# Optimization experiments

Hardware: AMD Instinct MI355X
Metric: run time of the kernel (lower is better)

## Reference

```python
import jax, jax.numpy as jnp
import numpy as np

# dims matching init_kwargs / input_specs
N, C, H, W = 8, 256, 64, 64
OUT_C, KH, KW = 256, 3, 3
STRIDE, PAD = 1, 1
OUT_H = (H - KH + 2 * PAD) // STRIDE + 1  # 64
OUT_W = (W - KW + 2 * PAD) // STRIDE + 1  # 64
K = KH * KW


def setup_inputs() -> dict:
    key = jax.random.key(0)
    k1, k2, k3 = jax.random.split(key, 3)
    x = jax.random.normal(k1, (N, C, H, W), dtype=jnp.float32)
    offset = jax.random.normal(k2, (N, 2 * K, OUT_H, OUT_W), dtype=jnp.float32)
    # kaiming-uniform-ish scale for weight (fan_in = C*KH*KW)
    bound = 1.0 / np.sqrt(C * KH * KW)
    weight = jax.random.uniform(k3, (OUT_C, C, KH, KW), dtype=jnp.float32,
                                minval=-bound, maxval=bound)
    return {"input": x, "offset": offset, "weight": weight}


def _deform_conv(x, offset, weight):
    # base sampling positions in pixel coords: y = oy*stride + ky - pad
    ky = jnp.repeat(jnp.arange(KH, dtype=jnp.float32) - PAD, KW)  # [K]
    kx = jnp.tile(jnp.arange(KW, dtype=jnp.float32) - PAD, KH)    # [K]
    oy = jnp.arange(OUT_H, dtype=jnp.float32) * STRIDE            # [outH]
    ox = jnp.arange(OUT_W, dtype=jnp.float32) * STRIDE            # [outW]
    base_y = ky[:, None, None] + oy[None, :, None]  # [K, outH, 1]
    base_x = kx[:, None, None] + ox[None, None, :]  # [K, 1, outW]

    off = offset.reshape(N, K, 2, OUT_H, OUT_W)
    y = base_y[None] + off[:, :, 0]  # [N, K, outH, outW], offset channel 0 = dy
    xp = base_x[None] + off[:, :, 1]  # channel 1 = dx

    # bilinear sample with zero padding (grid_sample align_corners=True, zeros)
    y0 = jnp.floor(y)
    x0 = jnp.floor(xp)
    bidx = jnp.arange(N)[:, None, None, None]
    acc = jnp.zeros((N, K, OUT_H, OUT_W, C), dtype=x.dtype)
    for dy in (0.0, 1.0):
        for dx in (0.0, 1.0):
            yi = y0 + dy
            xi = x0 + dx
            wgt = (1.0 - jnp.abs(y - yi)) * (1.0 - jnp.abs(xp - xi))
            valid = ((yi >= 0) & (yi <= H - 1) & (xi >= 0) & (xi <= W - 1))
            yc = jnp.clip(yi, 0, H - 1).astype(jnp.int32)
            xc = jnp.clip(xi, 0, W - 1).astype(jnp.int32)
            g = x[bidx, :, yc, xc]  # [N, K, outH, outW, C]
            acc = acc + g * (wgt * valid.astype(x.dtype))[..., None]

    # weight.view(outC, -1) flattens (C, KH, KW) -> (C, K) ordering
    w = weight.reshape(OUT_C, C, K)
    out = jnp.einsum('nkhwc,ock->nohw', acc, w)  # [N, outC, outH, outW]
    return out


def reference(input, offset, weight):
    # NOTE: original forward never adds bias -> faithfully omitted
    return _deform_conv(input, offset, weight)
```

## Files before the change

### kernel.cpp

```cpp
#include <hip/hip_runtime.h>
#include <hip/hip_fp16.h>
#include <stdint.h>


typedef _Float16 half8 __attribute__((ext_vector_type(8)));
typedef float f32x4 __attribute__((ext_vector_type(4)));

__device__ __forceinline__ __half2 h2(uint32_t u) {
  return __builtin_bit_cast(__half2, u);
}
__device__ __forceinline__ uint32_t packh2f(float a, float b) {
  return __builtin_bit_cast(uint32_t, __floats2half2_rn(a, b));
}
__device__ __forceinline__ __half2 duplo(uint32_t u) {
  return __half2half2(__builtin_bit_cast(__half, (unsigned short)(u & 0xffffu)));
}
__device__ __forceinline__ __half2 duphi(uint32_t u) {
  return __half2half2(__builtin_bit_cast(__half, (unsigned short)(u >> 16)));
}

__global__ __launch_bounds__(256) void prep_all_kernel(
    const float* __restrict__ x, const float* __restrict__ w,
    const float* __restrict__ offset,
    unsigned short* __restrict__ xb, unsigned short* __restrict__ w3s,
    unsigned short* __restrict__ coords) {
  __shared__ float tile[64][65];
  int tid = threadIdx.x;
  if (blockIdx.x < 2048) {
    int bn   = blockIdx.x >> 8;
    int rem  = blockIdx.x & 255;
    int y    = rem >> 2;
    int cblk = rem & 3;
    const float* src = x + ((size_t)(bn * 256 + cblk * 64)) * 4096 + y * 64;
#pragma unroll
    for (int i = 0; i < 4; ++i) {
      int u  = i * 256 + tid;
      int cl = u >> 4;
      int xs = (u & 15) * 4;
      float4 v = *(const float4*)(src + cl * 4096 + xs);
      tile[cl][xs] = v.x; tile[cl][xs + 1] = v.y;
      tile[cl][xs + 2] = v.z; tile[cl][xs + 3] = v.w;
    }
    __syncthreads();
    unsigned short* dst = xb + ((size_t)(bn * 64 + y) * 64) * 256 + cblk * 64;
#pragma unroll
    for (int i = 0; i < 8; ++i) {
      int v2  = i * 256 + tid;
      int xc  = v2 >> 5;
      int cl2 = (v2 & 31) * 2;
      *(uint32_t*)(dst + xc * 256 + cl2) = packh2f(tile[cl2][xc], tile[cl2 + 1][xc]);
    }
  } else if (blockIdx.x < 4352) {
    int idx = (blockIdx.x - 2048) * 256 + tid;
    int t    = idx >> 14;
    int r2   = idx & 16383;
    int e    = r2 & 7;
    int lane = (r2 >> 3) & 63;
    int ks   = (r2 >> 9) & 1;
    int nn   = (r2 >> 10) & 3;
    int wcol = (r2 >> 12) & 3;
    int oc = wcol * 64 + nn * 16 + (lane & 15);
    int kk = (ks * 4 + (lane >> 4)) * 8 + e;
    int c  = (t & 3) * 64 + kk;
    int k  = t >> 2;
    w3s[idx] = __builtin_bit_cast(unsigned short, __float2half(w[(oc * 256 + c) * 9 + k]));
  } else {
    int idx = (blockIdx.x - 4352) * 256 + tid;
    int ow  = idx & 63;
    int oh  = (idx >> 6) & 63;
    int r   = idx >> 12;
    int k   = r % 9;
    int bn  = r / 9;
    int ky = k / 3 - 1;
    int kx = k % 3 - 1;
    float offy = offset[((bn * 18 + 2 * k    ) * 64 + oh) * 64 + ow];
    float offx = offset[((bn * 18 + 2 * k + 1) * 64 + oh) * 64 + ow];
    float y = (float)(oh + ky) + offy;
    float x2 = (float)(ow + kx) + offx;
    float y0f = floorf(y), x0f = floorf(x2);
    float fy = y - y0f, fx = x2 - x0f;
    int y0 = (int)y0f, x0 = (int)x0f;
    int y1 = y0 + 1, x1 = x0 + 1;
    float vy0 = (y0 >= 0 && y0 <= 63) ? 1.0f : 0.0f;
    float vy1 = (y1 >= 0 && y1 <= 63) ? 1.0f : 0.0f;
    float vx0 = (x0 >= 0 && x0 <= 63) ? 1.0f : 0.0f;
    float vx1 = (x1 >= 0 && x1 <= 63) ? 1.0f : 0.0f;
    float wy0 = (1.0f - fy) * vy0, wy1 = fy * vy1;
    float wx0 = (1.0f - fx) * vx0, wx1 = fx * vx1;
    int y0c = min(max(y0, 0), 63), y1c = min(max(y1, 0), 63);
    int x0c = min(max(x0, 0), 63), x1c = min(max(x1, 0), 63);
    unsigned short ent[8];
    ent[0] = __builtin_bit_cast(unsigned short, __float2half(wy0 * wx0));
    ent[1] = __builtin_bit_cast(unsigned short, __float2half(wy0 * wx1));
    ent[2] = __builtin_bit_cast(unsigned short, __float2half(wy1 * wx0));
    ent[3] = __builtin_bit_cast(unsigned short, __float2half(wy1 * wx1));
    ent[4] = (unsigned short)(y0c * 64 + x0c);
    ent[5] = (unsigned short)(y0c * 64 + x1c);
    ent[6] = (unsigned short)(y1c * 64 + x0c);
    ent[7] = (unsigned short)(y1c * 64 + x1c);
    *(uint4*)(coords + (size_t)idx * 8) = *(const uint4*)ent;
  }
}

__global__ __launch_bounds__(512, 2) void deform_mfma_kernel(
    const unsigned short* __restrict__ xb,
    const unsigned short* __restrict__ coords,
    const unsigned short* __restrict__ w3s,
    float* __restrict__ out) {
  __shared__ __align__(16) unsigned short At[2][128 * 64];

  int bn  = blockIdx.x & 7;
  int ohp = blockIdx.x >> 3;
  int tid = threadIdx.x;

  int w    = tid >> 6;
  int lane = tid & 63;
  int wrow = w & 1;
  int wcol = w >> 1;
  int mrow = lane & 15;
  int quad = lane >> 4;

  int srow = tid >> 3;
  int sg   = tid & 7;

  const char* xbc = (const char*)(xb + (size_t)bn * (64 * 64 * 256));
  const unsigned short* cb0 = coords + ((size_t)((bn * 9) * 64 + ohp * 2) * 64 + srow) * 8;
  const unsigned short* cb1 = cb0 + 512;

  int aw0  = srow * 64 + ((sg ^ (srow & 7)) * 8);
  int grp0 = quad ^ (mrow & 7);
  int grp1 = (4 + quad) ^ (mrow & 7);
  int a_base = (wrow * 64 + mrow) * 64;
  int b_off  = wcol * 8192 + lane * 16;

  f32x4 acc[4][4] = {};
  half8 bA[2][4], bB[2][4];

  __half2 w00, w01, w02, w03, w10, w11, w12, w13;
  uint32_t o00, o01, o02, o03, o10, o11, o12, o13;
  uint4 cn0, cn1;
  uint4 ga0, ga1, ga2, ga3, gb0, gb1, gb2, gb3;

#define CBAR()                                                                  \
  {                                                                             \
    asm volatile("s_waitcnt lgkmcnt(0)" ::: "memory");                          \
    __builtin_amdgcn_s_barrier();                                               \
    asm volatile("" ::: "memory");                                              \
  }

#define BLOADR(TT, BS)                                                          \
  {                                                                             \
    const char* wp = (const char*)w3s + (size_t)(TT) * 32768 + b_off;           \
    _Pragma("unroll")                                                           \
    for (int nn = 0; nn < 4; ++nn) {                                            \
      BS[0][nn] = *(const half8*)(wp + (nn * 2 + 0) * 1024);                    \
      BS[1][nn] = *(const half8*)(wp + (nn * 2 + 1) * 1024);                    \
    }                                                                           \
  }

#define TAPSETUP_R(CE0, CE1)                                                    \
  {                                                                             \
    w00 = duplo((CE0).x); w01 = duphi((CE0).x);                                 \
    w02 = duplo((CE0).y); w03 = duphi((CE0).y);                                 \
    o00 = (((CE0).z & 0xffffu) << 9) + sg * 16;                                 \
    o01 = (((CE0).z >> 16) << 9) + sg * 16;                                     \
    o02 = (((CE0).w & 0xffffu) << 9) + sg * 16;                                 \
    o03 = (((CE0).w >> 16) << 9) + sg * 16;                                     \
    w10 = duplo((CE1).x); w11 = duphi((CE1).x);                                 \
    w12 = duplo((CE1).y); w13 = duphi((CE1).y);                                 \
    o10 = (((CE1).z & 0xffffu) << 9) + sg * 16;                                 \
    o11 = (((CE1).z >> 16) << 9) + sg * 16;                                     \
    o12 = (((CE1).w & 0xffffu) << 9) + sg * 16;                                 \
    o13 = (((CE1).w >> 16) << 9) + sg * 16;                                     \
  }

#define AGATHER(TT)                                                             \
  {                                                                             \
    ga0 = *(const uint4*)(xbc + o00 + ((TT) & 3) * 128);                        \
    ga1 = *(const uint4*)(xbc + o01 + ((TT) & 3) * 128);                        \
    ga2 = *(const uint4*)(xbc + o02 + ((TT) & 3) * 128);                        \
    ga3 = *(const uint4*)(xbc + o03 + ((TT) & 3) * 128);                        \
    gb0 = *(const uint4*)(xbc + o10 + ((TT) & 3) * 128);                        \
    gb1 = *(const uint4*)(xbc + o11 + ((TT) & 3) * 128);                        \
    gb2 = *(const uint4*)(xbc + o12 + ((TT) & 3) * 128);                        \
    gb3 = *(const uint4*)(xbc + o13 + ((TT) & 3) * 128);                        \
  }

#define AMATH(ATP)                                                              \
  {                                                                             \
    __half2 r0 = __hmul2(h2(ga0.x), w00);                                       \
    r0 = __hfma2(h2(ga1.x), w01, r0); r0 = __hfma2(h2(ga2.x), w02, r0);         \
    r0 = __hfma2(h2(ga3.x), w03, r0);                                           \
    __half2 r1 = __hmul2(h2(ga0.y), w00);                                       \
    r1 = __hfma2(h2(ga1.y), w01, r1); r1 = __hfma2(h2(ga2.y), w02, r1);         \
    r1 = __hfma2(h2(ga3.y), w03, r1);                                           \
    __half2 r2 = __hmul2(h2(ga0.z), w00);                                       \
    r2 = __hfma2(h2(ga1.z), w01, r2); r2 = __hfma2(h2(ga2.z), w02, r2);         \
    r2 = __hfma2(h2(ga3.z), w03, r2);                                           \
    __half2 r3 = __hmul2(h2(ga0.w), w00);                                       \
    r3 = __hfma2(h2(ga1.w), w01, r3); r3 = __hfma2(h2(ga2.w), w02, r3);         \
    r3 = __hfma2(h2(ga3.w), w03, r3);                                           \
    uint4 pk;                                                                   \
    pk.x = __builtin_bit_cast(uint32_t, r0);                                    \
    pk.y = __builtin_bit_cast(uint32_t, r1);                                    \
    pk.z = __builtin_bit_cast(uint32_t, r2);                                    \
    pk.w = __builtin_bit_cast(uint32_t, r3);                                    \
    *(uint4*)((ATP) + aw0) = pk;                                                \
    __half2 s0 = __hmul2(h2(gb0.x), w10);                                       \
    s0 = __hfma2(h2(gb1.x), w11, s0); s0 = __hfma2(h2(gb2.x), w12, s0);         \
    s0 = __hfma2(h2(gb3.x), w13, s0);                                           \
    __half2 s1 = __hmul2(h2(gb0.y), w10);                                       \
    s1 = __hfma2(h2(gb1.y), w11, s1); s1 = __hfma2(h2(gb2.y), w12, s1);         \
    s1 = __hfma2(h2(gb3.y), w13, s1);                                           \
    __half2 s2 = __hmul2(h2(gb0.z), w10);                                       \
    s2 = __hfma2(h2(gb1.z), w11, s2); s2 = __hfma2(h2(gb2.z), w12, s2);         \
    s2 = __hfma2(h2(gb3.z), w13, s2);                                           \
    __half2 s3 = __hmul2(h2(gb0.w), w10);                                       \
    s3 = __hfma2(h2(gb1.w), w11, s3); s3 = __hfma2(h2(gb2.w), w12, s3);         \
    s3 = __hfma2(h2(gb3.w), w13, s3);                                           \
    uint4 qk;                                                                   \
    qk.x = __builtin_bit_cast(uint32_t, s0);                                    \
    qk.y = __builtin_bit_cast(uint32_t, s1);                                    \
    qk.z = __builtin_bit_cast(uint32_t, s2);                                    \
    qk.w = __builtin_bit_cast(uint32_t, s3);                                    \
    *(uint4*)((ATP) + aw0 + 4096) = qk;                                         \
  }

#define COMPUTE(ATP, BS)                                                        \
  {                                                                             \
    __builtin_amdgcn_s_setprio(1);                                              \
    _Pragma("unroll")                                                           \
    for (int m = 0; m < 4; ++m) {                                               \
      half8 af0 = *(const half8*)((ATP) + a_base + m * 1024 + grp0 * 8);        \
      half8 af1 = *(const half8*)((ATP) + a_base + m * 1024 + grp1 * 8);        \
      _Pragma("unroll")                                                         \
      for (int nn = 0; nn < 4; ++nn) {                                          \
        acc[m][nn] = __builtin_amdgcn_mfma_f32_16x16x32_f16(af0, BS[0][nn], acc[m][nn], 0, 0, 0); \
        acc[m][nn] = __builtin_amdgcn_mfma_f32_16x16x32_f16(af1, BS[1][nn], acc[m][nn], 0, 0, 0); \
      }                                                                         \
    }                                                                           \
    __builtin_amdgcn_s_setprio(0);                                              \
  }

  {
    uint4 ce0 = *(const uint4*)cb0;
    uint4 ce1 = *(const uint4*)cb1;
    TAPSETUP_R(ce0, ce1)
  }
  AGATHER(0)
  BLOADR(0, bA)
  AMATH(&At[0][0])
  CBAR()

  for (int tap = 0; tap < 9; ++tap) {
#pragma unroll
    for (int cc = 0; cc < 4; ++cc) {
      const int t = tap * 4 + cc;
      if (t < 35) {
        if (cc == 3) TAPSETUP_R(cn0, cn1)
        AGATHER(t + 1)
        if (cc == 2 && tap < 8) {
          cn0 = *(const uint4*)(cb0 + (tap + 1) * 32768);
          cn1 = *(const uint4*)(cb1 + (tap + 1) * 32768);
        }
        if (cc & 1) { BLOADR(t + 1, bA) } else { BLOADR(t + 1, bB) }
      }
      if (cc & 1) { COMPUTE(&At[1][0], bB) } else { COMPUTE(&At[0][0], bA) }
      if (t < 35) {
        if (cc & 1) { AMATH(&At[0][0]) } else { AMATH(&At[1][0]) }
      }
      CBAR()
    }
  }

  float* outp = out + (size_t)bn * 256 * 4096 + (size_t)(ohp * 2 + wrow) * 64;
#pragma unroll
  for (int m = 0; m < 4; ++m) {
    int ow0 = m * 16 + quad * 4;
#pragma unroll
    for (int nn = 0; nn < 4; ++nn) {
      int oc = wcol * 64 + nn * 16 + mrow;
      *(f32x4*)(outp + (size_t)oc * 4096 + ow0) = acc[m][nn];
    }
  }
#undef CBAR
#undef BLOADR
#undef TAPSETUP_R
#undef AGATHER
#undef AMATH
#undef COMPUTE
}

extern "C" void kernel_launch(void* const* d_in, const int* in_sizes, int n_in,
                              void* d_out, int out_size, void* d_ws, size_t ws_size,
                              hipStream_t stream) {
  (void)in_sizes; (void)n_in; (void)out_size; (void)ws_size;
  const float* x      = (const float*)d_in[0];
  const float* offset = (const float*)d_in[1];
  const float* weight = (const float*)d_in[2];
  float* out = (float*)d_out;

  unsigned short* xb     = (unsigned short*)d_ws;
  unsigned short* w3s    = xb + (size_t)8 * 64 * 64 * 256;
  unsigned short* coords = w3s + (size_t)36 * 16384;

  prep_all_kernel<<<5504, 256, 0, stream>>>(x, weight, offset, xb, w3s, coords);
  deform_mfma_kernel<<<256, 512, 0, stream>>>(xb, coords, w3s, out);
}
```

Before: 140.7 us.

## Stage weight tiles into LDS via global_load_lds with double buffering

Weight (B) tiles were previously loaded straight from global memory into registers by every wave. They are now copied asynchronously into a double-buffered LDS tile with global_load_lds, each wave moving a slice, and then read from LDS into fragments just before the MFMAs. Explicit vmcnt waits replace the implicit register dependency. This removes redundant global traffic per wave and frees registers. In exchange it adds LDS reads, raises LDS usage (which may limit occupancy at 2 blocks per CU), and relies on the hand-counted vmcnt values being correct.

After: 149.9 us. 6.5% more time.

```diff
diff --git a/kernel.cpp b/kernel.cpp
--- a/kernel.cpp
+++ b/kernel.cpp
@@ -108,6 +108,7 @@
     const unsigned short* __restrict__ w3s,
     float* __restrict__ out) {
   __shared__ __align__(16) unsigned short At[2][128 * 64];
+  __shared__ __align__(16) unsigned short Bt[2][16384];
 
   int bn  = blockIdx.x & 7;
   int ohp = blockIdx.x >> 3;
@@ -131,10 +132,10 @@
   int grp0 = quad ^ (mrow & 7);
   int grp1 = (4 + quad) ^ (mrow & 7);
   int a_base = (wrow * 64 + mrow) * 64;
-  int b_off  = wcol * 8192 + lane * 16;
+  int b_off  = wcol * 4096 + lane * 8;
+  int d_off  = w * 2048 + lane * 8;
 
   f32x4 acc[4][4] = {};
-  half8 bA[2][4], bB[2][4];
 
   __half2 w00, w01, w02, w03, w10, w11, w12, w13;
   uint32_t o00, o01, o02, o03, o10, o11, o12, o13;
@@ -148,13 +149,16 @@
     asm volatile("" ::: "memory");                                              \
   }
 
-#define BLOADR(TT, BS)                                                          \
-  {                                                                             \
-    const char* wp = (const char*)w3s + (size_t)(TT) * 32768 + b_off;           \
+#define BDMA(TT, BB)                                                            \
+  {                                                                             \
+    const unsigned short* src = w3s + (size_t)(TT) * 16384 + d_off;             \
+    unsigned short* dst = &Bt[BB][0] + w * 2048;                                \
     _Pragma("unroll")                                                           \
-    for (int nn = 0; nn < 4; ++nn) {                                            \
-      BS[0][nn] = *(const half8*)(wp + (nn * 2 + 0) * 1024);                    \
-      BS[1][nn] = *(const half8*)(wp + (nn * 2 + 1) * 1024);                    \
+    for (int j = 0; j < 4; ++j) {                                               \
+      __builtin_amdgcn_global_load_lds(                                         \
+          (const __attribute__((address_space(1))) void*)(src + j * 512),       \
+          (__attribute__((address_space(3))) void*)(dst + j * 512),             \
+          16, 0, 0);                                                            \
     }                                                                           \
   }
 
@@ -226,8 +230,21 @@
     *(uint4*)((ATP) + aw0 + 4096) = qk;                                         \
   }
 
-#define COMPUTE(ATP, BS)                                                        \
-  {                                                                             \
+#define VMW(N)                                                                  \
+  {                                                                             \
+    asm volatile("s_waitcnt vmcnt(" #N ")" ::: "memory");                       \
+    __builtin_amdgcn_sched_barrier(0);                                          \
+  }
+
+#define COMPUTE(ATP, BTP, VM)                                                   \
+  {                                                                             \
+    VMW(VM)                                                                     \
+    half8 bfr[2][4];                                                            \
+    _Pragma("unroll")                                                           \
+    for (int nn = 0; nn < 4; ++nn) {                                            \
+      bfr[0][nn] = *(const half8*)((BTP) + b_off + (nn * 2 + 0) * 512);         \
+      bfr[1][nn] = *(const half8*)((BTP) + b_off + (nn * 2 + 1) * 512);         \
+    }                                                                           \
     __builtin_amdgcn_s_setprio(1);                                              \
     _Pragma("unroll")                                                           \
     for (int m = 0; m < 4; ++m) {                                               \
@@ -235,8 +252,8 @@
       half8 af1 = *(const half8*)((ATP) + a_base + m * 1024 + grp1 * 8);        \
       _Pragma("unroll")                                                         \
       for (int nn = 0; nn < 4; ++nn) {                                          \
-        acc[m][nn] = __builtin_amdgcn_mfma_f32_16x16x32_f16(af0, BS[0][nn], acc[m][nn], 0, 0, 0); \
-        acc[m][nn] = __builtin_amdgcn_mfma_f32_16x16x32_f16(af1, BS[1][nn], acc[m][nn], 0, 0, 0); \
+        acc[m][nn] = __builtin_amdgcn_mfma_f32_16x16x32_f16(af0, bfr[0][nn], acc[m][nn], 0, 0, 0); \
+        acc[m][nn] = __builtin_amdgcn_mfma_f32_16x16x32_f16(af1, bfr[1][nn], acc[m][nn], 0, 0, 0); \
       }                                                                         \
     }                                                                           \
     __builtin_amdgcn_s_setprio(0);                                              \
@@ -248,7 +265,7 @@
     TAPSETUP_R(ce0, ce1)
   }
   AGATHER(0)
-  BLOADR(0, bA)
+  BDMA(0, 0)
   AMATH(&At[0][0])
   CBAR()
 
@@ -259,13 +276,19 @@
       if (t < 35) {
         if (cc == 3) TAPSETUP_R(cn0, cn1)
         AGATHER(t + 1)
+        if (cc & 1) { BDMA(t + 1, 0) } else { BDMA(t + 1, 1) }
         if (cc == 2 && tap < 8) {
           cn0 = *(const uint4*)(cb0 + (tap + 1) * 32768);
           cn1 = *(const uint4*)(cb1 + (tap + 1) * 32768);
         }
-        if (cc & 1) { BLOADR(t + 1, bA) } else { BLOADR(t + 1, bB) }
       }
-      if (cc & 1) { COMPUTE(&At[1][0], bB) } else { COMPUTE(&At[0][0], bA) }
+      if (cc & 1) {
+        if (t == 35) { COMPUTE(&At[1][0], &Bt[1][0], 0) }
+        else         { COMPUTE(&At[1][0], &Bt[1][0], 12) }
+      } else {
+        if (cc == 2 && tap < 8) { COMPUTE(&At[0][0], &Bt[0][0], 14) }
+        else                    { COMPUTE(&At[0][0], &Bt[0][0], 12) }
+      }
       if (t < 35) {
         if (cc & 1) { AMATH(&At[0][0]) } else { AMATH(&At[1][0]) }
       }
@@ -284,10 +307,11 @@
     }
   }
 #undef CBAR
-#undef BLOADR
+#undef BDMA
 #undef TAPSETUP_R
 #undef AGATHER
 #undef AMATH
+#undef VMW
 #undef COMPUTE
 }
 
```
